# Performance work log

Measured on AMD Instinct MI355X. Metric: run time of the kernel, lower is better.

## Reference

```python
import jax, jax.numpy as jnp
import numpy as np

L = 4        # num_blocks
D = 512      # d_model
H = 8        # num_heads
DFF = 2048   # d_ff
EPS = 1.1920929e-07  # torch RMSNorm default eps = finfo(fp32).eps


def setup_inputs() -> dict:
    key = jax.random.key(0)
    ks = jax.random.split(key, 12)
    B, S = 4, 1024
    s = 0.02
    return {
        "x": jax.random.normal(ks[0], (B, S, D), jnp.float32),
        "col_ids": jax.random.randint(ks[1], (B, S), 0, 32),
        "row_ids": jax.random.randint(ks[2], (B, S), 0, 128),
        "nbr_ids": jax.random.randint(ks[3], (B, S), 0, 64),
        # per-block, per-relation attention weights (nn.Linear: y = x @ W.T)
        "Wq": jax.random.normal(ks[4], (L, 4, D, D), jnp.float32) * s,
        "Wk": jax.random.normal(ks[5], (L, 4, D, D), jnp.float32) * s,
        "Wv": jax.random.normal(ks[6], (L, 4, D, D), jnp.float32) * s,
        "Wo": jax.random.normal(ks[7], (L, 4, D, D), jnp.float32) * s,
        # SwiGLU FFN weights per block
        "W1": jax.random.normal(ks[8], (L, DFF, D), jnp.float32) * s,
        "W3": jax.random.normal(ks[9], (L, DFF, D), jnp.float32) * s,
        "W2": jax.random.normal(ks[10], (L, D, DFF), jnp.float32) * s,
        # RMSNorm scales: 4 attn norms + 1 ffn norm per block + final norm_out
        "g_attn": jnp.ones((L, 4, D), jnp.float32),
        "g_ffn": jnp.ones((L, D), jnp.float32),
        "g_out": jnp.ones((D,), jnp.float32),
    }


def _rms(x, g):
    return x * jax.lax.rsqrt(jnp.mean(x * x, axis=-1, keepdims=True) + EPS) * g


def _attn(x, wq, wk, wv, wo, mask):
    # x: [B,S,D]; mask: [B,S,S] bool (True = attend) or None for full attention
    B, S, _ = x.shape
    hd = D // H
    scale = 1.0 / np.sqrt(hd).astype(np.float32)
    q = (x @ wq.T).reshape(B, S, H, hd).transpose(0, 2, 1, 3)  # bhsd
    k = (x @ wk.T).reshape(B, S, H, hd).transpose(0, 2, 1, 3)
    v = (x @ wv.T).reshape(B, S, H, hd).transpose(0, 2, 1, 3)
    sc = jnp.einsum('bhqd,bhkd->bhqk', q, k) * scale
    if mask is not None:
        sc = jnp.where(mask[:, None, :, :], sc, jnp.float32(-1e30))
    a = jax.nn.softmax(sc, axis=-1)
    o = jnp.einsum('bhqk,bhkd->bhqd', a, v).transpose(0, 2, 1, 3).reshape(B, S, D)
    return o @ wo.T


def reference(x, col_ids, row_ids, nbr_ids, Wq, Wk, Wv, Wo, W1, W3, W2, g_attn, g_ffn, g_out):
    # relation order in RelationalBlock: col, feat, nbr, full
    masks = [ids[:, :, None] == ids[:, None, :] for ids in (col_ids, row_ids, nbr_ids)] + [None]
    for l in range(L):
        for r in range(4):
            x = x + _attn(_rms(x, g_attn[l, r]), Wq[l, r], Wk[l, r], Wv[l, r], Wo[l, r], masks[r])
        h = _rms(x, g_ffn[l])
        x = x + (jax.nn.silu(h @ W1[l].T) * (h @ W3[l].T)) @ W2[l].T
    return _rms(x, g_out)
```

## Files before the change

### kernel.cpp

```cpp
#include <hip/hip_runtime.h>
#include <hip/hip_bf16.h>


typedef __attribute__((ext_vector_type(4))) float f32x4;
typedef __attribute__((ext_vector_type(8))) short s16x8;
typedef __attribute__((ext_vector_type(4))) short s16x4;

#define SEQ 1024
#define DM 512
#define MTOT 4096
#define EPSV 1.1920929e-07f
#define LOG2E 1.44269504088896f

static __device__ __forceinline__ float b2f(short s) {
  unsigned u = ((unsigned)(unsigned short)s) << 16;
  return __builtin_bit_cast(float, u);
}
static __device__ __forceinline__ short f2b(float f) {
  unsigned u = __builtin_bit_cast(unsigned, f);
  u = (u + 0x7fffu + ((u >> 16) & 1u)) >> 16;
  return (short)(unsigned short)u;
}

#define MFMA_BF16(a, b, c) __builtin_amdgcn_mfma_f32_16x16x32_bf16((a), (b), (c), 0, 0, 0)
#define GLLDS(gp, lp)                                                                        \
  __builtin_amdgcn_global_load_lds((const __attribute__((address_space(1))) unsigned*)(gp),  \
                                   (__attribute__((address_space(3))) unsigned*)(lp), 16, 0, 0)
#define GLLDS4(gp, lp)                                                                       \
  __builtin_amdgcn_global_load_lds((const __attribute__((address_space(1))) unsigned*)(gp),  \
                                   (__attribute__((address_space(3))) unsigned*)(lp), 4, 0, 0)

__global__ void cvt_place(const f32x4* __restrict__ src, s16x4* __restrict__ dst, int n4,
                          int shift, int stride4, int off4, float scale) {
  int i = blockIdx.x * 256 + threadIdx.x;
  if (i >= n4) return;
  f32x4 v = src[i];
  s16x4 o;
  o[0] = f2b(v[0] * scale); o[1] = f2b(v[1] * scale);
  o[2] = f2b(v[2] * scale); o[3] = f2b(v[3] * scale);
  int c = i >> shift, r = i & ((1 << shift) - 1);
  dst[(size_t)c * stride4 + off4 + r] = o;
}

__global__ void cvt_w13(const f32x4* __restrict__ src, s16x4* __restrict__ dst, int n4, int off) {
  int i = blockIdx.x * 256 + threadIdx.x;
  if (i >= n4) return;
  f32x4 v = src[i];
  s16x4 o;
  o[0] = f2b(v[0]); o[1] = f2b(v[1]); o[2] = f2b(v[2]); o[3] = f2b(v[3]);
  int srcrow = i >> 7, r = i & 127;
  int l = srcrow >> 11, n = srcrow & 2047;
  int dstrow = l * 4096 + n * 2 + off;
  dst[(size_t)dstrow * 128 + r] = o;
}

template<bool F32OUT>
__global__ void rmsnorm_kernel(const float* __restrict__ x, const float* __restrict__ g,
                               void* __restrict__ outp) {
  int row = blockIdx.x * 4 + (threadIdx.x >> 6);
  int lane = threadIdx.x & 63;
  const float* xr = x + (size_t)row * DM + lane * 8;
  f32x4 a = *(const f32x4*)xr;
  f32x4 b = *(const f32x4*)(xr + 4);
  float ss = a[0]*a[0]+a[1]*a[1]+a[2]*a[2]+a[3]*a[3]+b[0]*b[0]+b[1]*b[1]+b[2]*b[2]+b[3]*b[3];
#pragma unroll
  for (int m = 1; m < 64; m <<= 1) ss += __shfl_xor(ss, m, 64);
  float sc = rsqrtf(ss * (1.0f / DM) + EPSV);
  const float* gp = g + lane * 8;
  if (F32OUT) {
    float* o = (float*)outp + (size_t)row * DM + lane * 8;
    f32x4 o0, o1;
#pragma unroll
    for (int j = 0; j < 4; j++) { o0[j] = a[j] * sc * gp[j]; o1[j] = b[j] * sc * gp[4 + j]; }
    *(f32x4*)o = o0;
    *(f32x4*)(o + 4) = o1;
  } else {
    s16x8 o;
#pragma unroll
    for (int j = 0; j < 4; j++) { o[j] = f2b(a[j] * sc * gp[j]); o[4 + j] = f2b(b[j] * sc * gp[4 + j]); }
    *(s16x8*)((short*)outp + (size_t)row * DM + lane * 8) = o;
  }
}

template<int AR, int AC, int FUSE>
__global__ __launch_bounds__(256) void gemm_bt(const short* __restrict__ A, const short* __restrict__ W,
                                               short* __restrict__ outb, float* __restrict__ outf,
                                               short* __restrict__ vtb, int N, int K) {
  constexpr int BM = AR * 32;
  constexpr int BN = AC * 32;
  constexpr int NA = BM / 64, NB = BN / 64;
  constexpr int LPS = NA + NB;
  __shared__ short As[2][BM * 32];
  __shared__ short Bs[2][BN * 32];
  const int tid = threadIdx.x;
  const int lane = tid & 63;
  const int w = tid >> 6;
  const int wr = w >> 1, wc = w & 1;
  const int qi = lane & 15, g = lane >> 4;
  const int m0 = blockIdx.x * BM, n0 = blockIdx.y * BN;

  const short* ap[NA];
  const short* wp[NB];
#pragma unroll
  for (int i = 0; i < NA; i++) {
    int s = i * 256 + tid;
    int row = s >> 2, gl = s & 3, gd = gl ^ ((row >> 1) & 3);
    ap[i] = A + (size_t)(m0 + row) * K + gd * 8;
  }
#pragma unroll
  for (int i = 0; i < NB; i++) {
    int s = i * 256 + tid;
    int row = s >> 2, gl = s & 3, gd = gl ^ ((row >> 1) & 3);
    wp[i] = W + (size_t)(n0 + row) * K + gd * 8;
  }
  int aro[AR], bro[AC];
#pragma unroll
  for (int i = 0; i < AR; i++) {
    int row = wr * AR * 16 + i * 16 + qi;
    aro[i] = row * 64 + ((g ^ ((row >> 1) & 3)) * 16);
  }
#pragma unroll
  for (int j = 0; j < AC; j++) {
    int row = wc * AC * 16 + j * 16 + qi;
    bro[j] = row * 64 + ((g ^ ((row >> 1) & 3)) * 16);
  }
  f32x4 acc[AR][AC] = {};

#define STAGE_G(BUF)                                                             \
  {                                                                              \
    _Pragma("unroll")                                                            \
    for (int i = 0; i < NA; i++) {                                               \
      GLLDS(ap[i], (char*)As[BUF] + (i * 256 + w * 64) * 16);                    \
      ap[i] += 32;                                                               \
    }                                                                            \
    _Pragma("unroll")                                                            \
    for (int i = 0; i < NB; i++) {                                               \
      GLLDS(wp[i], (char*)Bs[BUF] + (i * 256 + w * 64) * 16);                    \
      wp[i] += 32;                                                               \
    }                                                                            \
  }

#define BODY_G(BUF, T)                                                           \
  {                                                                              \
    s16x8 af[AR], bf[AC];                                                        \
    _Pragma("unroll")                                                            \
    for (int i = 0; i < AR; i++) af[i] = *(const s16x8*)((char*)As[BUF] + aro[i]); \
    _Pragma("unroll")                                                            \
    for (int j = 0; j < AC; j++) bf[j] = *(const s16x8*)((char*)Bs[BUF] + bro[j]); \
    asm volatile("s_waitcnt lgkmcnt(0)" ::: "memory");                           \
    __builtin_amdgcn_s_barrier();                                                \
    bool more = ((T) + 2 < nt);                                                  \
    if (more) STAGE_G(BUF);                                                      \
    _Pragma("unroll")                                                            \
    for (int i = 0; i < AR; i++)                                                 \
      _Pragma("unroll")                                                          \
      for (int j = 0; j < AC; j++)                                               \
        acc[i][j] = MFMA_BF16(af[i], bf[j], acc[i][j]);                          \
    if (more) asm volatile("s_waitcnt vmcnt(%0)" :: "n"(LPS) : "memory");        \
    else      asm volatile("s_waitcnt vmcnt(0)" ::: "memory");                   \
    __builtin_amdgcn_s_barrier();                                                \
  }

  const int nt = K >> 5;
  STAGE_G(0);
  STAGE_G(1);
  asm volatile("s_waitcnt vmcnt(%0)" :: "n"(LPS) : "memory");
  __builtin_amdgcn_s_barrier();
  for (int t = 0; t < nt; t += 2) {
    BODY_G(0, t);
    BODY_G(1, t + 1);
  }
#undef STAGE_G
#undef BODY_G

#pragma unroll
  for (int i = 0; i < AR; i++) {
    int rbase = m0 + wr * AR * 16 + i * 16 + g * 4;
#pragma unroll
    for (int j = 0; j < AC; j++) {
      int col = n0 + wc * AC * 16 + j * 16 + qi;
      if (FUSE == 2 && col >= 1024) {
        int bbv = rbase >> 10, s = rbase & 1023;
        int c = col - 1024, hhv = c >> 6, d = c & 63;
        int o = (s & 63) >> 2;
        int gg = o & 3, h2 = (o >> 2) & 1, q32 = o >> 3;
        int pnew = q32 * 8 + gg * 2 + h2;
        s16x4 o4;
#pragma unroll
        for (int r = 0; r < 4; r++) o4[r] = f2b(acc[i][j][r]);
        *(s16x4*)(vtb + (((size_t)(bbv * 8 + hhv) * 64 + d) << 10) + (s & ~63) + pnew * 4) = o4;
      } else if (FUSE == 3) {
#pragma unroll
        for (int r = 0; r < 4; r++) {
          float own = acc[i][j][r];
          float other = __shfl_xor(own, 1, 64);
          float sv = own / (1.0f + __expf(-own));
          if (!(lane & 1))
            outb[(size_t)(rbase + r) * (N >> 1) + (col >> 1)] = f2b(sv * other);
        }
      } else {
#pragma unroll
        for (int r = 0; r < 4; r++) {
          size_t idx = (size_t)(rbase + r) * N + col;
          if (FUSE == 1) outf[idx] += acc[i][j][r];
          else           outb[idx] = f2b(acc[i][j][r]);
        }
      }
    }
  }
}

__global__ __launch_bounds__(256) void attn_kernel(const short* __restrict__ qkv, const short* __restrict__ vt,
                                                   const int* __restrict__ ids, short* __restrict__ Ob) {
  const int bh = blockIdx.x;
  const int bb = bh >> 3, hh = bh & 7;
  const int q0 = blockIdx.y * 64;
  const int tid = threadIdx.x, lane = tid & 63, w = tid >> 6;
  const int g = lane >> 4, qi = lane & 15;
  __shared__ short Kl[2][128 * 64];
  __shared__ short Vl[2][64 * 128];
  __shared__ int Kid[2][128];
  const short* kbase = qkv + 512 + hh * 64;
  const short* vbase = vt + (size_t)bh * 64 * SEQ;
  s16x8 qf0, qf1;
  {
    int qrow = q0 + w * 16 + qi;
    const short* qp = qkv + (size_t)(bb * SEQ + qrow) * 1536 + hh * 64 + g * 8;
    qf0 = *(const s16x8*)qp;
    qf1 = *(const s16x8*)(qp + 32);
  }
  int qid = 0;
  if (ids) qid = ids[bb * SEQ + q0 + w * 16 + qi];
  float m_ = -1e30f, l_ = 0.f;
  f32x4 oacc[4] = {};

#define STAGE_ATTN(buf, ktt)                                                                     \
  {                                                                                              \
    _Pragma("unroll")                                                                            \
    for (int i = 0; i < 4; i++) {                                                                \
      int s = i * 256 + tid;                                                                     \
      int row = s >> 3, gl = s & 7, gd = gl ^ (row & 7);                                         \
      GLLDS(kbase + (size_t)(bb * SEQ + (ktt) + row) * 1536 + gd * 8,                            \
            (char*)Kl[buf] + (i * 256 + w * 64) * 16);                                           \
    }                                                                                            \
    _Pragma("unroll")                                                                            \
    for (int i = 0; i < 4; i++) {                                                                \
      int s = i * 256 + tid;                                                                     \
      int d = s >> 4, gl = s & 15, gd = gl ^ (d & 7);                                            \
      GLLDS(vbase + (size_t)d * SEQ + (ktt) + gd * 8, (char*)Vl[buf] + (i * 256 + w * 64) * 16); \
    }                                                                                            \
    if (ids && w < 2) GLLDS4(ids + bb * SEQ + (ktt) + w * 64 + lane, (char*)Kid[buf] + w * 256); \
  }

  STAGE_ATTN(0, 0);
  __syncthreads();
  int cur = 0;
  for (int kt = 0; kt < SEQ; kt += 128) {
    if (kt + 128 < SEQ) STAGE_ATTN(cur ^ 1, kt + 128);
    f32x4 sc[8];
#pragma unroll
    for (int kc = 0; kc < 8; kc++) {
      int krow = kc * 16 + qi;
      s16x8 kf0 = *(const s16x8*)(Kl[cur] + krow * 64 + ((g ^ (krow & 7)) * 8));
      s16x8 kf1 = *(const s16x8*)(Kl[cur] + krow * 64 + (((4 + g) ^ (krow & 7)) * 8));
      f32x4 s4 = {};
      s4 = MFMA_BF16(kf0, qf0, s4);
      s4 = MFMA_BF16(kf1, qf1, s4);
      sc[kc] = s4;
    }
    float p[8][4];
#pragma unroll
    for (int kc = 0; kc < 8; kc++)
#pragma unroll
      for (int r = 0; r < 4; r++) p[kc][r] = sc[kc][r];
    if (ids) {
#pragma unroll
      for (int kc = 0; kc < 8; kc++) {
        int4 kid4 = *(const int4*)(Kid[cur] + kc * 16 + g * 4);
        if (kid4.x != qid) p[kc][0] = -1e30f;
        if (kid4.y != qid) p[kc][1] = -1e30f;
        if (kid4.z != qid) p[kc][2] = -1e30f;
        if (kid4.w != qid) p[kc][3] = -1e30f;
      }
    }
    float mx = fmaxf(fmaxf(p[0][0], p[0][1]), fmaxf(p[0][2], p[0][3]));
#pragma unroll
    for (int kc = 1; kc < 8; kc++)
      mx = fmaxf(mx, fmaxf(fmaxf(p[kc][0], p[kc][1]), fmaxf(p[kc][2], p[kc][3])));
    mx = fmaxf(mx, __shfl_xor(mx, 16, 64));
    mx = fmaxf(mx, __shfl_xor(mx, 32, 64));
    if (__any(mx > m_ + 8.f)) {
      float nm = fmaxf(m_, mx);
      float c = exp2f(m_ - nm);
      m_ = nm;
      l_ *= c;
#pragma unroll
      for (int r = 0; r < 4; r++) {
        float cr = __shfl(c, g * 4 + r, 16);
        oacc[0][r] *= cr; oacc[1][r] *= cr; oacc[2][r] *= cr; oacc[3][r] *= cr;
      }
    }
    float sum = 0.f;
#pragma unroll
    for (int kc = 0; kc < 8; kc++)
#pragma unroll
      for (int r = 0; r < 4; r++) {
        p[kc][r] = exp2f(p[kc][r] - m_);
        sum += p[kc][r];
      }
    sum += __shfl_xor(sum, 16, 64);
    sum += __shfl_xor(sum, 32, 64);
    l_ += sum;
#pragma unroll
    for (int kk = 0; kk < 2; kk++) {
      s16x8 pa, pb;
#pragma unroll
      for (int r = 0; r < 4; r++) {
        pa[r] = f2b(p[kk * 4 + 0][r]); pa[4 + r] = f2b(p[kk * 4 + 1][r]);
        pb[r] = f2b(p[kk * 4 + 2][r]); pb[4 + r] = f2b(p[kk * 4 + 3][r]);
      }
#pragma unroll
      for (int dt = 0; dt < 4; dt++) {
        int dl = dt * 16 + qi;
        const short* vr = Vl[cur] + dl * 128;
        s16x8 vf0 = *(const s16x8*)(vr + (kk * 8 + (g ^ (dl & 7))) * 8);
        s16x8 vf1 = *(const s16x8*)(vr + (kk * 8 + ((4 + g) ^ (dl & 7))) * 8);
        oacc[dt] = MFMA_BF16(pa, vf0, oacc[dt]);
        oacc[dt] = MFMA_BF16(pb, vf1, oacc[dt]);
      }
    }
    __syncthreads();
    cur ^= 1;
  }
#undef STAGE_ATTN
  const size_t obase = (size_t)(bb * SEQ) * DM + hh * 64;
#pragma unroll
  for (int r = 0; r < 4; r++) {
    float lr = __shfl(l_, g * 4 + r, 16);
    float inv = 1.0f / lr;
    int q = q0 + w * 16 + g * 4 + r;
#pragma unroll
    for (int dt = 0; dt < 4; dt++)
      Ob[obase + (size_t)q * DM + dt * 16 + qi] = f2b(oacc[dt][r] * inv);
  }
}

extern "C" void kernel_launch(void* const* d_in, const int* in_sizes, int n_in,
                              void* d_out, int out_size, void* d_ws, size_t ws_size,
                              hipStream_t stream) {
  const float* x_in  = (const float*)d_in[0];
  const int* col_ids = (const int*)d_in[1];
  const int* row_ids = (const int*)d_in[2];
  const int* nbr_ids = (const int*)d_in[3];
  const float* g_attn = (const float*)d_in[11];
  const float* g_ffn  = (const float*)d_in[12];
  const float* g_out  = (const float*)d_in[13];

  char* ws = (char*)d_ws;
  float* x   = (float*)(ws);
  short* h   = (short*)(ws + (size_t)(8u  << 20));
  short* qkv = (short*)(ws + (size_t)(12u << 20));
  short* vt  = (short*)(ws + (size_t)(24u << 20));
  short* ob  = (short*)(ws + (size_t)(28u << 20));
  short* fa  = (short*)(ws + (size_t)(44u << 20));
  short* wqkv = (short*)(ws + (size_t)(60u  << 20));
  short* wob  = (short*)(ws + (size_t)(84u  << 20));
  short* w13  = (short*)(ws + (size_t)(92u  << 20));
  short* w2b  = (short*)(ws + (size_t)(108u << 20));

  const int N4 = 1048576;
  cvt_place<<<4096, 256, 0, stream>>>((const f32x4*)d_in[4], (s16x4*)wqkv, N4, 16, 196608, 0, 0.125f * LOG2E);
  cvt_place<<<4096, 256, 0, stream>>>((const f32x4*)d_in[5], (s16x4*)wqkv, N4, 16, 196608, 65536, 1.0f);
  cvt_place<<<4096, 256, 0, stream>>>((const f32x4*)d_in[6], (s16x4*)wqkv, N4, 16, 196608, 131072, 1.0f);
  cvt_place<<<4096, 256, 0, stream>>>((const f32x4*)d_in[7], (s16x4*)wob,  N4, 20, 0, 0, 1.0f);
  cvt_w13<<<4096, 256, 0, stream>>>((const f32x4*)d_in[8], (s16x4*)w13, N4, 0);
  cvt_w13<<<4096, 256, 0, stream>>>((const f32x4*)d_in[9], (s16x4*)w13, N4, 1);
  cvt_place<<<4096, 256, 0, stream>>>((const f32x4*)d_in[10], (s16x4*)w2b, N4, 20, 0, 0, 1.0f);

  hipMemcpyAsync(x, x_in, (size_t)MTOT * DM * 4, hipMemcpyDeviceToDevice, stream);

  const int* idsarr[4] = {col_ids, row_ids, nbr_ids, nullptr};

  for (int l = 0; l < 4; l++) {
    for (int r = 0; r < 4; r++) {
      rmsnorm_kernel<false><<<1024, 256, 0, stream>>>(x, g_attn + (size_t)(l * 4 + r) * DM, (void*)h);
      size_t woff = (size_t)(l * 4 + r) * 1536 * DM;
      gemm_bt<4, 2, 2><<<dim3(32, 24), 256, 0, stream>>>(h, wqkv + woff, qkv, nullptr, vt, 1536, DM);
      attn_kernel<<<dim3(32, 16), 256, 0, stream>>>(qkv, vt, idsarr[r], ob);
      gemm_bt<2, 2, 1><<<dim3(64, 8), 256, 0, stream>>>(ob, wob + (size_t)(l * 4 + r) * DM * DM,
                                                        nullptr, x, nullptr, DM, DM);
    }
    rmsnorm_kernel<false><<<1024, 256, 0, stream>>>(x, g_ffn + (size_t)l * DM, (void*)h);
    gemm_bt<4, 2, 3><<<dim3(32, 64), 256, 0, stream>>>(h, w13 + (size_t)l * 4096 * DM, fa, nullptr, nullptr, 4096, DM);
    gemm_bt<2, 2, 1><<<dim3(64, 8), 256, 0, stream>>>(fa, w2b + (size_t)l * DM * 2048, nullptr, x, nullptr, DM, 2048);
  }
  rmsnorm_kernel<true><<<1024, 256, 0, stream>>>(x, g_out, d_out);
}
```

Before: 1.139 ms.

## Fuse RMSNorm into GEMM epilogues via folded gains and atomic row sums

The RMSNorm gain vectors are folded into the bf16 QKV and W1/W3 weights during conversion. Residual GEMMs now write x, a raw bf16 copy h, and per-row sum-of-squares through atomics. The following QKV or FFN GEMM then scales its output rows by rsqrt of that sum, so the 20 standalone rmsnorm launches disappear. The seven conversion kernels are also merged into one launch. The cost is one atomic per row segment, and normalising after the matmul on unnormalised bf16 input changes rounding.

```diff
diff --git a/kernel.cpp b/kernel.cpp
--- a/kernel.cpp
+++ b/kernel.cpp
@@ -30,33 +30,69 @@
   __builtin_amdgcn_global_load_lds((const __attribute__((address_space(1))) unsigned*)(gp),  \
                                    (__attribute__((address_space(3))) unsigned*)(lp), 4, 0, 0)
 
-__global__ void cvt_place(const f32x4* __restrict__ src, s16x4* __restrict__ dst, int n4,
-                          int shift, int stride4, int off4, float scale) {
+__global__ void cvt_all(const f32x4* __restrict__ wq, const f32x4* __restrict__ wk,
+                        const f32x4* __restrict__ wv, const f32x4* __restrict__ wo,
+                        const f32x4* __restrict__ w1, const f32x4* __restrict__ w3,
+                        const f32x4* __restrict__ w2, const float* __restrict__ g_attn,
+                        const float* __restrict__ g_ffn, s16x4* __restrict__ wqkv,
+                        s16x4* __restrict__ wob, s16x4* __restrict__ w13,
+                        s16x4* __restrict__ w2b) {
   int i = blockIdx.x * 256 + threadIdx.x;
-  if (i >= n4) return;
-  f32x4 v = src[i];
+  int which = blockIdx.y;
   s16x4 o;
-  o[0] = f2b(v[0] * scale); o[1] = f2b(v[1] * scale);
-  o[2] = f2b(v[2] * scale); o[3] = f2b(v[3] * scale);
-  int c = i >> shift, r = i & ((1 << shift) - 1);
-  dst[(size_t)c * stride4 + off4 + r] = o;
-}
-
-__global__ void cvt_w13(const f32x4* __restrict__ src, s16x4* __restrict__ dst, int n4, int off) {
-  int i = blockIdx.x * 256 + threadIdx.x;
-  if (i >= n4) return;
-  f32x4 v = src[i];
-  s16x4 o;
-  o[0] = f2b(v[0]); o[1] = f2b(v[1]); o[2] = f2b(v[2]); o[3] = f2b(v[3]);
-  int srcrow = i >> 7, r = i & 127;
-  int l = srcrow >> 11, n = srcrow & 2047;
-  int dstrow = l * 4096 + n * 2 + off;
-  dst[(size_t)dstrow * 128 + r] = o;
-}
-
-template<bool F32OUT>
-__global__ void rmsnorm_kernel(const float* __restrict__ x, const float* __restrict__ g,
-                               void* __restrict__ outp) {
+  if (which < 3) {
+    const f32x4* src = which == 0 ? wq : (which == 1 ? wk : wv);
+    f32x4 v = src[i];
+    int lr = i >> 16, k4 = i & 127, n = (i >> 7) & 511;
+    const float* gp = g_attn + lr * 512 + k4 * 4;
+    float sc = (which == 0) ? 0.125f * LOG2E : 1.0f;
+#pragma unroll
+    for (int j = 0; j < 4; j++) o[j] = f2b(v[j] * gp[j] * sc);
+    wqkv[(size_t)lr * 196608 + (which * 512 + n) * 128 + k4] = o;
+  } else if (which == 3) {
+    f32x4 v = wo[i];
+#pragma unroll
+    for (int j = 0; j < 4; j++) o[j] = f2b(v[j]);
+    wob[i] = o;
+  } else if (which < 6) {
+    const f32x4* src = which == 4 ? w1 : w3;
+    int off = which - 4;
+    f32x4 v = src[i];
+    int l = i >> 18, n = (i >> 7) & 2047, k4 = i & 127;
+    const float* gp = g_ffn + l * 512 + k4 * 4;
+#pragma unroll
+    for (int j = 0; j < 4; j++) o[j] = f2b(v[j] * gp[j]);
+    w13[(size_t)l * 524288 + (n * 2 + off) * 128 + k4] = o;
+  } else {
+    f32x4 v = w2[i];
+#pragma unroll
+    for (int j = 0; j < 4; j++) o[j] = f2b(v[j]);
+    w2b[i] = o;
+  }
+}
+
+__global__ void init_kernel(const float* __restrict__ xin, float* __restrict__ x,
+                            short* __restrict__ h, float* __restrict__ ssq) {
+  int row = blockIdx.x * 4 + (threadIdx.x >> 6);
+  int lane = threadIdx.x & 63;
+  const float* xr = xin + (size_t)row * DM + lane * 8;
+  f32x4 a = *(const f32x4*)xr;
+  f32x4 b = *(const f32x4*)(xr + 4);
+  float* xo = x + (size_t)row * DM + lane * 8;
+  *(f32x4*)xo = a;
+  *(f32x4*)(xo + 4) = b;
+  s16x8 ho;
+#pragma unroll
+  for (int j = 0; j < 4; j++) { ho[j] = f2b(a[j]); ho[4 + j] = f2b(b[j]); }
+  *(s16x8*)(h + (size_t)row * DM + lane * 8) = ho;
+  float ss = a[0]*a[0]+a[1]*a[1]+a[2]*a[2]+a[3]*a[3]+b[0]*b[0]+b[1]*b[1]+b[2]*b[2]+b[3]*b[3];
+#pragma unroll
+  for (int m = 1; m < 64; m <<= 1) ss += __shfl_xor(ss, m, 64);
+  if (lane == 0) ssq[row] = ss;
+}
+
+__global__ void rmsnorm_out(const float* __restrict__ x, const float* __restrict__ g,
+                            float* __restrict__ outp) {
   int row = blockIdx.x * 4 + (threadIdx.x >> 6);
   int lane = threadIdx.x & 63;
   const float* xr = x + (size_t)row * DM + lane * 8;
@@ -67,25 +103,21 @@
   for (int m = 1; m < 64; m <<= 1) ss += __shfl_xor(ss, m, 64);
   float sc = rsqrtf(ss * (1.0f / DM) + EPSV);
   const float* gp = g + lane * 8;
-  if (F32OUT) {
-    float* o = (float*)outp + (size_t)row * DM + lane * 8;
-    f32x4 o0, o1;
-#pragma unroll
-    for (int j = 0; j < 4; j++) { o0[j] = a[j] * sc * gp[j]; o1[j] = b[j] * sc * gp[4 + j]; }
-    *(f32x4*)o = o0;
-    *(f32x4*)(o + 4) = o1;
-  } else {
-    s16x8 o;
-#pragma unroll
-    for (int j = 0; j < 4; j++) { o[j] = f2b(a[j] * sc * gp[j]); o[4 + j] = f2b(b[j] * sc * gp[4 + j]); }
-    *(s16x8*)((short*)outp + (size_t)row * DM + lane * 8) = o;
-  }
+  float* o = outp + (size_t)row * DM + lane * 8;
+  f32x4 o0, o1;
+#pragma unroll
+  for (int j = 0; j < 4; j++) { o0[j] = a[j] * sc * gp[j]; o1[j] = b[j] * sc * gp[4 + j]; }
+  *(f32x4*)o = o0;
+  *(f32x4*)(o + 4) = o1;
 }
 
 template<int AR, int AC, int FUSE>
 __global__ __launch_bounds__(256) void gemm_bt(const short* __restrict__ A, const short* __restrict__ W,
                                                short* __restrict__ outb, float* __restrict__ outf,
-                                               short* __restrict__ vtb, int N, int K) {
+                                               short* __restrict__ vtb,
+                                               const float* __restrict__ ssq_in,
+                                               float* __restrict__ ssq_out,
+                                               short* __restrict__ hb, int N, int K) {
   constexpr int BM = AR * 32;
   constexpr int BN = AC * 32;
   constexpr int NA = BM / 64, NB = BN / 64;
@@ -173,6 +205,24 @@
 #undef STAGE_G
 #undef BODY_G
 
+  float srow[AR][4];
+  if (FUSE == 2 || FUSE == 3) {
+#pragma unroll
+    for (int i = 0; i < AR; i++) {
+      int rbase = m0 + wr * AR * 16 + i * 16 + g * 4;
+#pragma unroll
+      for (int r = 0; r < 4; r++)
+        srow[i][r] = rsqrtf(ssq_in[rbase + r] * (1.0f / DM) + EPSV);
+    }
+  }
+  float part[AR][4];
+  if (FUSE == 1) {
+#pragma unroll
+    for (int i = 0; i < AR; i++)
+#pragma unroll
+      for (int r = 0; r < 4; r++) part[i][r] = 0.f;
+  }
+
 #pragma unroll
   for (int i = 0; i < AR; i++) {
     int rbase = m0 + wr * AR * 16 + i * 16 + g * 4;
@@ -187,24 +237,43 @@
         int pnew = q32 * 8 + gg * 2 + h2;
         s16x4 o4;
 #pragma unroll
-        for (int r = 0; r < 4; r++) o4[r] = f2b(acc[i][j][r]);
+        for (int r = 0; r < 4; r++) o4[r] = f2b(acc[i][j][r] * srow[i][r]);
         *(s16x4*)(vtb + (((size_t)(bbv * 8 + hhv) * 64 + d) << 10) + (s & ~63) + pnew * 4) = o4;
       } else if (FUSE == 3) {
 #pragma unroll
         for (int r = 0; r < 4; r++) {
-          float own = acc[i][j][r];
+          float own = acc[i][j][r] * srow[i][r];
           float other = __shfl_xor(own, 1, 64);
           float sv = own / (1.0f + __expf(-own));
           if (!(lane & 1))
             outb[(size_t)(rbase + r) * (N >> 1) + (col >> 1)] = f2b(sv * other);
         }
-      } else {
+      } else if (FUSE == 1) {
 #pragma unroll
         for (int r = 0; r < 4; r++) {
           size_t idx = (size_t)(rbase + r) * N + col;
-          if (FUSE == 1) outf[idx] += acc[i][j][r];
-          else           outb[idx] = f2b(acc[i][j][r]);
+          float xnew = outf[idx] + acc[i][j][r];
+          outf[idx] = xnew;
+          hb[idx] = f2b(xnew);
+          part[i][r] += xnew * xnew;
         }
+      } else {
+#pragma unroll
+        for (int r = 0; r < 4; r++)
+          outb[(size_t)(rbase + r) * N + col] = f2b(acc[i][j][r] * srow[i][r]);
+      }
+    }
+  }
+  if (FUSE == 1) {
+#pragma unroll
+    for (int i = 0; i < AR; i++) {
+      int rbase = m0 + wr * AR * 16 + i * 16 + g * 4;
+#pragma unroll
+      for (int r = 0; r < 4; r++) {
+        float p = part[i][r];
+#pragma unroll
+        for (int m = 1; m < 16; m <<= 1) p += __shfl_xor(p, m, 16);
+        if (qi == 0) atomicAdd(&ssq_out[rbase + r], p);
       }
     }
   }
@@ -357,42 +426,47 @@
   const float* g_out  = (const float*)d_in[13];
 
   char* ws = (char*)d_ws;
-  float* x   = (float*)(ws);
-  short* h   = (short*)(ws + (size_t)(8u  << 20));
-  short* qkv = (short*)(ws + (size_t)(12u << 20));
-  short* vt  = (short*)(ws + (size_t)(24u << 20));
-  short* ob  = (short*)(ws + (size_t)(28u << 20));
-  short* fa  = (short*)(ws + (size_t)(44u << 20));
+  float* x    = (float*)(ws);
+  short* h    = (short*)(ws + (size_t)(8u  << 20));
+  short* qkv  = (short*)(ws + (size_t)(12u << 20));
+  short* vt   = (short*)(ws + (size_t)(24u << 20));
+  short* ob   = (short*)(ws + (size_t)(28u << 20));
+  float* sbuf = (float*)(ws + (size_t)(33u << 20));
+  short* fa   = (short*)(ws + (size_t)(44u << 20));
   short* wqkv = (short*)(ws + (size_t)(60u  << 20));
   short* wob  = (short*)(ws + (size_t)(84u  << 20));
   short* w13  = (short*)(ws + (size_t)(92u  << 20));
   short* w2b  = (short*)(ws + (size_t)(108u << 20));
 
-  const int N4 = 1048576;
-  cvt_place<<<4096, 256, 0, stream>>>((const f32x4*)d_in[4], (s16x4*)wqkv, N4, 16, 196608, 0, 0.125f * LOG2E);
-  cvt_place<<<4096, 256, 0, stream>>>((const f32x4*)d_in[5], (s16x4*)wqkv, N4, 16, 196608, 65536, 1.0f);
-  cvt_place<<<4096, 256, 0, stream>>>((const f32x4*)d_in[6], (s16x4*)wqkv, N4, 16, 196608, 131072, 1.0f);
-  cvt_place<<<4096, 256, 0, stream>>>((const f32x4*)d_in[7], (s16x4*)wob,  N4, 20, 0, 0, 1.0f);
-  cvt_w13<<<4096, 256, 0, stream>>>((const f32x4*)d_in[8], (s16x4*)w13, N4, 0);
-  cvt_w13<<<4096, 256, 0, stream>>>((const f32x4*)d_in[9], (s16x4*)w13, N4, 1);
-  cvt_place<<<4096, 256, 0, stream>>>((const f32x4*)d_in[10], (s16x4*)w2b, N4, 20, 0, 0, 1.0f);
-
-  hipMemcpyAsync(x, x_in, (size_t)MTOT * DM * 4, hipMemcpyDeviceToDevice, stream);
+  hipMemsetAsync(sbuf, 0, 21 * 4096 * sizeof(float), stream);
+  cvt_all<<<dim3(4096, 7), 256, 0, stream>>>((const f32x4*)d_in[4], (const f32x4*)d_in[5],
+                                             (const f32x4*)d_in[6], (const f32x4*)d_in[7],
+                                             (const f32x4*)d_in[8], (const f32x4*)d_in[9],
+                                             (const f32x4*)d_in[10], g_attn, g_ffn,
+                                             (s16x4*)wqkv, (s16x4*)wob, (s16x4*)w13, (s16x4*)w2b);
+  init_kernel<<<1024, 256, 0, stream>>>(x_in, x, h, sbuf);
 
   const int* idsarr[4] = {col_ids, row_ids, nbr_ids, nullptr};
 
   for (int l = 0; l < 4; l++) {
     for (int r = 0; r < 4; r++) {
-      rmsnorm_kernel<false><<<1024, 256, 0, stream>>>(x, g_attn + (size_t)(l * 4 + r) * DM, (void*)h);
+      int slot = l * 5 + r;
       size_t woff = (size_t)(l * 4 + r) * 1536 * DM;
-      gemm_bt<4, 2, 2><<<dim3(32, 24), 256, 0, stream>>>(h, wqkv + woff, qkv, nullptr, vt, 1536, DM);
+      gemm_bt<4, 2, 2><<<dim3(32, 24), 256, 0, stream>>>(h, wqkv + woff, qkv, nullptr, vt,
+                                                         sbuf + (size_t)slot * 4096, nullptr,
+                                                         nullptr, 1536, DM);
       attn_kernel<<<dim3(32, 16), 256, 0, stream>>>(qkv, vt, idsarr[r], ob);
       gemm_bt<2, 2, 1><<<dim3(64, 8), 256, 0, stream>>>(ob, wob + (size_t)(l * 4 + r) * DM * DM,
-                                                        nullptr, x, nullptr, DM, DM);
-    }
-    rmsnorm_kernel<false><<<1024, 256, 0, stream>>>(x, g_ffn + (size_t)l * DM, (void*)h);
-    gemm_bt<4, 2, 3><<<dim3(32, 64), 256, 0, stream>>>(h, w13 + (size_t)l * 4096 * DM, fa, nullptr, nullptr, 4096, DM);
-    gemm_bt<2, 2, 1><<<dim3(64, 8), 256, 0, stream>>>(fa, w2b + (size_t)l * DM * 2048, nullptr, x, nullptr, DM, 2048);
-  }
-  rmsnorm_kernel<true><<<1024, 256, 0, stream>>>(x, g_out, d_out);
-}
+                                                        nullptr, x, nullptr, nullptr,
+                                                        sbuf + (size_t)(slot + 1) * 4096, h, DM, DM);
+    }
+    int fslot = l * 5 + 4;
+    gemm_bt<4, 2, 3><<<dim3(32, 64), 256, 0, stream>>>(h, w13 + (size_t)l * 4096 * DM, fa, nullptr,
+                                                       nullptr, sbuf + (size_t)fslot * 4096,
+                                                       nullptr, nullptr, 4096, DM);
+    gemm_bt<2, 2, 1><<<dim3(64, 8), 256, 0, stream>>>(fa, w2b + (size_t)l * DM * 2048, nullptr, x,
+                                                      nullptr, nullptr,
+                                                      sbuf + (size_t)(fslot + 1) * 4096, h, DM, 2048);
+  }
+  rmsnorm_out<<<1024, 256, 0, stream>>>(x, g_out, (float*)d_out);
+}
```

Result: no change. 1.134 ms (-0.4%).
